# Optimization experiments

Hardware: AMD Instinct MI355X
Metric: run time of the kernel (lower is better)

## Reference

```python
import jax, jax.numpy as jnp
import numpy as np

D_MODEL = 2048
N_HEADS = 32
N_KV = 8
D_HEAD = D_MODEL // N_HEADS  # 64
GROUP = N_HEADS // N_KV      # 4
B, T = 2, 4096
WINDOW = 1024
SINK = 4
ROPE_BASE = 10000.0


def _rope(x, start_pos=0):
    # x: [b, h, t, d]; Llama-style rotate-half RoPE
    t, d = x.shape[2], x.shape[3]
    pos = jnp.arange(start_pos, start_pos + t, dtype=jnp.float32)
    inv_freq = 1.0 / (ROPE_BASE ** (jnp.arange(0, d, 2, dtype=jnp.float32) / d))
    ang = pos[:, None] * inv_freq            # [t, d/2]
    cos, sin = jnp.cos(ang), jnp.sin(ang)
    x1, x2 = jnp.split(x, 2, axis=-1)
    return jnp.concatenate([x1 * cos - x2 * sin, x2 * cos + x1 * sin], axis=-1)


def setup_inputs() -> dict:
    key = jax.random.key(0)
    ks = jax.random.split(key, 5)
    x = jax.random.normal(ks[0], (B, T, D_MODEL), jnp.float32)
    wq = jax.random.normal(ks[1], (D_MODEL, D_MODEL), jnp.float32) * 0.02
    wk = jax.random.normal(ks[2], (N_KV * D_HEAD, D_MODEL), jnp.float32) * 0.02
    wv = jax.random.normal(ks[3], (N_KV * D_HEAD, D_MODEL), jnp.float32) * 0.02
    w_proj = jax.random.normal(ks[4], (D_MODEL, D_MODEL), jnp.float32) * 0.02
    return {"x": x, "wq": wq, "wk": wk, "wv": wv, "w_proj": w_proj}


def reference(x, wq, wk, wv, w_proj):
    b, t, _ = x.shape
    # QKV projections (Linear, no bias): y = x @ W^T, split into heads -> [b,h,t,d]
    q = (x @ wq.T).reshape(b, t, N_HEADS, D_HEAD).transpose(0, 2, 1, 3)
    k = (x @ wk.T).reshape(b, t, N_KV, D_HEAD).transpose(0, 2, 1, 3)
    v = (x @ wv.T).reshape(b, t, N_KV, D_HEAD).transpose(0, 2, 1, 3)
    q = _rope(q, 0)
    k = _rope(k, 0)
    # sliding window + attention sink KV slicing (tokens > window + sink)
    if t > WINDOW + SINK:
        k = jnp.concatenate([k[:, :, :SINK], k[:, :, -WINDOW:]], axis=2)
        v = jnp.concatenate([v[:, :, :SINK], v[:, :, -WINDOW:]], axis=2)
    # repeat_kv: 'b h t d -> b (h group) t d'
    k = jnp.repeat(k, GROUP, axis=1)
    v = jnp.repeat(v, GROUP, axis=1)
    s = k.shape[2]
    scores = jnp.einsum("bhtd,bhsd->bhts", q, k) / np.float32(np.sqrt(D_HEAD))
    # torch SDPA is_causal: top-left aligned tril(L, S)
    causal = jnp.arange(s)[None, :] <= jnp.arange(t)[:, None]  # [t, s]
    scores = jnp.where(causal[None, None], scores, jnp.float32(-1e30))
    probs = jax.nn.softmax(scores, axis=-1)
    ctx = jnp.einsum("bhts,bhsd->bhtd", probs, v)
    ctx = ctx.transpose(0, 2, 1, 3).reshape(b, t, D_MODEL)
    return ctx @ w_proj.T
```

## Files before the change

kernel.cpp:

```cpp
#include <hip/hip_runtime.h>

#define D_MODEL 2048
#define N_HEADS 32
#define N_KV    8
#define D_HEAD  64
#define BATCH   2
#define TLEN    4096
#define WINDOW  1024
#define SINK    4
#define SEQ_S   (WINDOW + SINK)
#define S_PADN  1088
#define MROWS   (BATCH * TLEN)
#define KV_DIM  512
#define KV_STR  1024
#define LOG2E   1.44269504088896340736f
#define PSP     72

typedef __bf16 bf16_t;
typedef __attribute__((ext_vector_type(8))) __bf16 bf16x8;
typedef __attribute__((ext_vector_type(4))) __bf16 bf16x4;
typedef __attribute__((ext_vector_type(4))) float   f32x4;

__device__ __forceinline__ void load_lds16(const void* g, void* l) {
  __builtin_amdgcn_global_load_lds(
      (__attribute__((address_space(1))) void*)g,
      (__attribute__((address_space(3))) void*)l, 16, 0, 0);
}

__global__ __launch_bounds__(256) void cvt_f32_bf16(const float* __restrict__ src,
                                                    bf16_t* __restrict__ dst, int n)
{
  int i = ((int)blockIdx.x * 256 + (int)threadIdx.x) * 4;
  if (i >= n) return;
  const float4 v = *(const float4*)(src + i);
  bf16x4 o;
  o[0] = (bf16_t)v.x; o[1] = (bf16_t)v.y; o[2] = (bf16_t)v.z; o[3] = (bf16_t)v.w;
  *(bf16x4*)(dst + i) = o;
}

template <typename OutT>
__global__ __launch_bounds__(256) void gemm_bt(const bf16_t* __restrict__ A,
                                               const bf16_t* __restrict__ W,
                                               OutT* __restrict__ C,
                                               int M, int N, int K)
{
  __shared__ __align__(16) bf16_t As[128 * 32];
  __shared__ __align__(16) bf16_t Bs[128 * 32];
  const int tid  = threadIdx.x;
  const int lane = tid & 63;
  const int wave = tid >> 6;
  const int quad = lane >> 4;
  const int col  = lane & 15;
  const int wm   = (wave >> 1) * 64;
  const int wn   = (wave & 1) * 64;
  const int bm   = blockIdx.x * 128;
  const int bn   = blockIdx.y * 128;

  const int e0 = tid, e1 = 256 + tid;
  const int r0 = e0 >> 2, c0 = ((e0 & 3) ^ (r0 & 3)) * 8;
  const int r1 = e1 >> 2, c1 = ((e1 & 3) ^ (r1 & 3)) * 8;
  const bf16_t* gA0 = A + (size_t)(bm + r0) * K + c0;
  const bf16_t* gA1 = A + (size_t)(bm + r1) * K + c1;
  const bf16_t* gB0 = W + (size_t)(bn + r0) * K + c0;
  const bf16_t* gB1 = W + (size_t)(bn + r1) * K + c1;
  char* lA0 = (char*)As + wave * 1024;
  char* lA1 = (char*)As + 4096 + wave * 1024;
  char* lB0 = (char*)Bs + wave * 1024;
  char* lB1 = (char*)Bs + 4096 + wave * 1024;

  f32x4 acc[4][4] = {};

  for (int k0 = 0; k0 < K; k0 += 32) {
    __syncthreads();
    load_lds16(gA0 + k0, lA0);
    load_lds16(gA1 + k0, lA1);
    load_lds16(gB0 + k0, lB0);
    load_lds16(gB1 + k0, lB1);
    __syncthreads();
    bf16x8 af[4], bfr[4];
    for (int i = 0; i < 4; ++i) {
      int row = wm + i * 16 + col;
      af[i] = *(const bf16x8*)((const char*)As + row * 64 + ((quad ^ (row & 3)) * 16));
    }
    for (int j = 0; j < 4; ++j) {
      int row = wn + j * 16 + col;
      bfr[j] = *(const bf16x8*)((const char*)Bs + row * 64 + ((quad ^ (row & 3)) * 16));
    }
    for (int i = 0; i < 4; ++i)
      for (int j = 0; j < 4; ++j)
        acc[i][j] = __builtin_amdgcn_mfma_f32_16x16x32_bf16(af[i], bfr[j], acc[i][j], 0, 0, 0);
  }

  for (int i = 0; i < 4; ++i)
    for (int j = 0; j < 4; ++j)
      for (int r = 0; r < 4; ++r) {
        size_t row = (size_t)(bm + wm + i * 16 + quad * 4 + r);
        size_t cc  = (size_t)(bn + wn + j * 16 + col);
        C[row * N + cc] = (OutT)acc[i][j][r];
      }
}

__global__ __launch_bounds__(256) void rope_kernel(bf16_t* __restrict__ q,
                                                   bf16_t* __restrict__ kv)
{
  const size_t QP = (size_t)MROWS * N_HEADS * 32;
  const size_t KP = (size_t)MROWS * N_KV * 32;
  size_t idx = (size_t)blockIdx.x * 256 + threadIdx.x;
  bf16_t* base;
  int i, h, rowlen;
  size_t m;
  if (idx < QP) {
    i = (int)(idx & 31);
    size_t hm = idx >> 5;
    h = (int)(hm & (N_HEADS - 1));
    m = hm >> 5;
    base = q; rowlen = D_MODEL;
  } else {
    idx -= QP;
    if (idx >= KP) return;
    i = (int)(idx & 31);
    size_t hm = idx >> 5;
    h = (int)(hm & (N_KV - 1));
    m = hm >> 3;
    base = kv; rowlen = KV_STR;
  }
  int t = (int)(m & (TLEN - 1));
  float inv = __builtin_exp2f(-(float)i * (13.287712379549449f / 32.0f));
  float ang = (float)t * inv;
  float sn, cs;
  sincosf(ang, &sn, &cs);
  size_t off = m * (size_t)rowlen + (size_t)h * D_HEAD + i;
  float x1 = (float)base[off];
  float x2 = (float)base[off + 32];
  base[off]      = (bf16_t)(x1 * cs - x2 * sn);
  base[off + 32] = (bf16_t)(x2 * cs + x1 * sn);
}

__global__ __launch_bounds__(256) void transpose_v(const bf16_t* __restrict__ KV,
                                                   bf16_t* __restrict__ Vt)
{
  __shared__ __align__(16) bf16_t tile[32][72];
  const int tid = threadIdx.x;
  const int s0  = blockIdx.x * 32;
  const int bk  = blockIdx.y;
  const int b   = bk >> 3, kvh = bk & 7;
  {
    int srow = tid >> 3;
    int dcol = (tid & 7) * 8;
    int sg = s0 + srow;
    int orig = (sg < SINK) ? sg : sg + (TLEN - WINDOW - SINK);
    if (orig > TLEN - 1) orig = TLEN - 1;
    const bf16_t* src = KV + (size_t)(b * TLEN + orig) * KV_STR + KV_DIM + kvh * D_HEAD + dcol;
    *(bf16x8*)&tile[srow][dcol] = *(const bf16x8*)src;
  }
  __syncthreads();
  {
    int d  = tid >> 2;
    int sc = (tid & 3) * 8;
    bf16x8 v;
    for (int j = 0; j < 8; ++j) v[j] = tile[sc + j][d];
    *(bf16x8*)(Vt + (size_t)(bk * 64 + d) * S_PADN + s0 + sc) = v;
  }
}

__global__ __launch_bounds__(256, 3) void attn_kernel(const bf16_t* __restrict__ Q,
                                                      const bf16_t* __restrict__ KV,
                                                      const bf16_t* __restrict__ Vt,
                                                      bf16_t* __restrict__ ctx)
{
  __shared__ __align__(16) bf16_t Ks[2][64 * 64];
  __shared__ __align__(16) bf16_t Vs[2][64 * 64];
  __shared__ __align__(16) bf16_t Ps[4][32 * PSP];
  __shared__ float Lt[4][32];
  const int tid = threadIdx.x, lane = tid & 63, wave = tid >> 6;
  const int quad = lane >> 4, col = lane & 15;
  const int bh = blockIdx.y, b = bh >> 5, h = bh & 31, kvh = h >> 2;
  const int bkv = b * 8 + kvh;
  const int t0b = blockIdx.x * 128;
  const int tw0 = t0b + wave * 32;

  bf16x8 qf[2][2];
  for (int g = 0; g < 2; ++g) {
    const bf16_t* qrow = Q + (size_t)(b * TLEN + tw0 + g * 16 + col) * D_MODEL + h * D_HEAD;
    for (int c = 0; c < 2; ++c) {
      bf16x8 v = *(const bf16x8*)(qrow + c * 32 + quad * 8);
      for (int i = 0; i < 8; ++i) v[i] = (bf16_t)((float)v[i] * (0.125f * LOG2E));
      qf[g][c] = v;
    }
  }

  f32x4 oAcc[2][4] = {};
  float lsum[2] = {0.f, 0.f};

  const int s_end  = (t0b + 128 < SEQ_S) ? t0b + 128 : SEQ_S;
  const int nsteps = (s_end + 63) >> 6;

  auto stage = [&](int st, int buf) {
    const int sb = st * 64;
#pragma unroll
    for (int kk = 0; kk < 2; ++kk) {
      int e = kk * 256 + tid;
      int srow = e >> 3;
      int cb = (e & 7) ^ (srow & 7);
      int sg = sb + srow;
      int orig = (sg < SINK) ? sg : sg + (TLEN - WINDOW - SINK);
      if (orig > TLEN - 1) orig = TLEN - 1;
      const bf16_t* gk = KV + (size_t)(b * TLEN + orig) * KV_STR + kvh * D_HEAD + cb * 8;
      load_lds16(gk, (char*)&Ks[buf][0] + kk * 4096 + wave * 1024);
      const bf16_t* gv = Vt + (size_t)(bkv * 64 + srow) * S_PADN + sb + cb * 8;
      load_lds16(gv, (char*)&Vs[buf][0] + kk * 4096 + wave * 1024);
    }
  };

  stage(0, 0);
  for (int st = 0; st < nsteps; ++st) {
    const int cur = st & 1;
    const int s0 = st * 64;
    const bool dead = (s0 > tw0 + 31);
    const bool full = (s0 + 63 <= tw0) && (s0 + 63 < SEQ_S);
    __syncthreads();

    if (!dead) {
      f32x4 sacc[4][2] = {};
#pragma unroll
      for (int c = 0; c < 2; ++c) {
#pragma unroll
        for (int mt = 0; mt < 4; ++mt) {
          int rr = mt * 16 + col;
          const bf16x8 kf = *(const bf16x8*)((const char*)&Ks[cur][0] + rr * 128 +
                                             ((((c << 2) | quad) ^ (col & 7)) * 16));
          sacc[mt][0] = __builtin_amdgcn_mfma_f32_16x16x32_bf16(kf, qf[0][c], sacc[mt][0], 0, 0, 0);
          sacc[mt][1] = __builtin_amdgcn_mfma_f32_16x16x32_bf16(kf, qf[1][c], sacc[mt][1], 0, 0, 0);
        }
      }
#pragma unroll
      for (int g = 0; g < 2; ++g) {
        const int t = tw0 + g * 16 + col;
#pragma unroll
        for (int mt = 0; mt < 4; ++mt) {
          bf16x4 pk;
          float ls = 0.f;
#pragma unroll
          for (int r = 0; r < 4; ++r) {
            float p = __builtin_exp2f(sacc[mt][g][r]);
            if (!full) {
              int s = s0 + mt * 16 + quad * 4 + r;
              p = (s <= t && s < SEQ_S) ? p : 0.0f;
            }
            ls += p;
            pk[r] = (bf16_t)p;
          }
          lsum[g] += ls;
          *(bf16x4*)(&Ps[wave][(g * 16 + col) * PSP + mt * 16 + quad * 4]) = pk;
        }
      }
    }
    __syncthreads();
    if (st + 1 < nsteps) stage(st + 1, cur ^ 1);

    if (!dead) {
      bf16x8 pf[2][2];
#pragma unroll
      for (int g = 0; g < 2; ++g)
#pragma unroll
        for (int c = 0; c < 2; ++c)
          pf[g][c] = *(const bf16x8*)(&Ps[wave][(g * 16 + col) * PSP + c * 32 + quad * 8]);
#pragma unroll
      for (int c = 0; c < 2; ++c) {
#pragma unroll
        for (int nj = 0; nj < 4; ++nj) {
          int rr = nj * 16 + col;
          const bf16x8 vf = *(const bf16x8*)((const char*)&Vs[cur][0] + rr * 128 +
                                             ((((c << 2) | quad) ^ (col & 7)) * 16));
          oAcc[0][nj] = __builtin_amdgcn_mfma_f32_16x16x32_bf16(pf[0][c], vf, oAcc[0][nj], 0, 0, 0);
          oAcc[1][nj] = __builtin_amdgcn_mfma_f32_16x16x32_bf16(pf[1][c], vf, oAcc[1][nj], 0, 0, 0);
        }
      }
    }
  }

  for (int g = 0; g < 2; ++g) {
    lsum[g] += __shfl_xor(lsum[g], 16, 64);
    lsum[g] += __shfl_xor(lsum[g], 32, 64);
  }
  if (quad == 0) { Lt[wave][col] = lsum[0]; Lt[wave][16 + col] = lsum[1]; }
  __syncthreads();

#pragma unroll
  for (int g = 0; g < 2; ++g) {
    float rli[4];
#pragma unroll
    for (int r = 0; r < 4; ++r)
      rli[r] = __builtin_amdgcn_rcpf(Lt[wave][g * 16 + quad * 4 + r]);
#pragma unroll
    for (int nj = 0; nj < 4; ++nj)
#pragma unroll
      for (int r = 0; r < 4; ++r) {
        size_t row = (size_t)(b * TLEN + tw0 + g * 16 + quad * 4 + r);
        ctx[row * D_MODEL + h * D_HEAD + nj * 16 + col] = (bf16_t)(oAcc[g][nj][r] * rli[r]);
      }
  }
}

extern "C" void kernel_launch(void* const* d_in, const int* in_sizes, int n_in,
                              void* d_out, int out_size, void* d_ws, size_t ws_size,
                              hipStream_t stream)
{
  const float* x  = (const float*)d_in[0];
  const float* wq = (const float*)d_in[1];
  const float* wk = (const float*)d_in[2];
  const float* wv = (const float*)d_in[3];
  const float* wp = (const float*)d_in[4];

  const int NX  = MROWS * D_MODEL;
  const int NWQ = D_MODEL * D_MODEL;
  const int NWK = KV_DIM * D_MODEL;

  bf16_t* xb    = (bf16_t*)d_ws;
  bf16_t* wqb   = xb  + (size_t)NX;
  bf16_t* wkb   = wqb + (size_t)NWQ;
  bf16_t* wvb   = wkb + (size_t)NWK;
  bf16_t* wpb   = wvb + (size_t)NWK;
  bf16_t* q_buf = wpb + (size_t)NWQ;
  bf16_t* kv_buf = q_buf + (size_t)NX;
  bf16_t* vt_buf = kv_buf + (size_t)MROWS * KV_STR;
  bf16_t* c_buf  = xb;
  float*  out    = (float*)d_out;

  cvt_f32_bf16<<<NX  / 1024, 256, 0, stream>>>(x,  xb,  NX);
  cvt_f32_bf16<<<NWQ / 1024, 256, 0, stream>>>(wq, wqb, NWQ);
  cvt_f32_bf16<<<NWK / 1024, 256, 0, stream>>>(wk, wkb, NWK);
  cvt_f32_bf16<<<NWK / 1024, 256, 0, stream>>>(wv, wvb, NWK);
  cvt_f32_bf16<<<NWQ / 1024, 256, 0, stream>>>(wp, wpb, NWQ);

  gemm_bt<bf16_t><<<dim3(MROWS / 128, D_MODEL / 128), 256, 0, stream>>>(xb, wqb, q_buf, MROWS, D_MODEL, D_MODEL);
  gemm_bt<bf16_t><<<dim3(MROWS / 128, KV_STR / 128), 256, 0, stream>>>(xb, wkb, kv_buf, MROWS, KV_STR, D_MODEL);

  {
    size_t total = (size_t)MROWS * N_HEADS * 32 + (size_t)MROWS * N_KV * 32;
    rope_kernel<<<(unsigned)((total + 255) / 256), 256, 0, stream>>>(q_buf, kv_buf);
  }
  transpose_v<<<dim3(S_PADN / 32, BATCH * N_KV), 256, 0, stream>>>(kv_buf, vt_buf);
  attn_kernel<<<dim3(TLEN / 128, BATCH * N_HEADS), 256, 0, stream>>>(q_buf, kv_buf, vt_buf, c_buf);
  gemm_bt<float><<<dim3(MROWS / 128, D_MODEL / 128), 256, 0, stream>>>(c_buf, wpb, out, MROWS, D_MODEL, D_MODEL);
}
```

Measured before the change: 557.7 us.

## Fuse Q RoPE into attention, merge converts, stream V from global

Five fp32-to-bf16 conversion launches are merged into one kernel. Q RoPE moves into the attention kernel's Q-fragment load, so the standalone RoPE pass only touches K. Inside attention, V fragments are read straight from global memory instead of being staged in LDS. The row-sum is computed with an MFMA against a ones vector, which removes the shuffle/LDS reduction and one barrier per step, and occupancy is raised to 4 blocks. The risks are extra sincos work per attention block and uncached global V reads whose latency may not be hidden.

```diff
diff --git a/kernel.cpp b/kernel.cpp
--- a/kernel.cpp
+++ b/kernel.cpp
@@ -27,12 +27,27 @@
       (__attribute__((address_space(3))) void*)l, 16, 0, 0);
 }
 
-__global__ __launch_bounds__(256) void cvt_f32_bf16(const float* __restrict__ src,
-                                                    bf16_t* __restrict__ dst, int n)
-{
-  int i = ((int)blockIdx.x * 256 + (int)threadIdx.x) * 4;
-  if (i >= n) return;
-  const float4 v = *(const float4*)(src + i);
+#define NX  (MROWS * D_MODEL)
+#define NWQ (D_MODEL * D_MODEL)
+#define NWK (KV_DIM * D_MODEL)
+#define NALL (NX + 2 * NWQ + 2 * NWK)
+
+__global__ __launch_bounds__(256) void cvt_all(const float* __restrict__ x,
+                                               const float* __restrict__ wq,
+                                               const float* __restrict__ wk,
+                                               const float* __restrict__ wv,
+                                               const float* __restrict__ wp,
+                                               bf16_t* __restrict__ dst)
+{
+  long i = ((long)blockIdx.x * 256 + threadIdx.x) * 4;
+  const float* src;
+  long off;
+  if (i < NX)                          { src = x;  off = i; }
+  else if (i < NX + NWQ)               { src = wq; off = i - NX; }
+  else if (i < NX + NWQ + NWK)         { src = wk; off = i - NX - NWQ; }
+  else if (i < NX + NWQ + 2L * NWK)    { src = wv; off = i - NX - NWQ - NWK; }
+  else                                 { src = wp; off = i - NX - NWQ - 2L * NWK; }
+  const float4 v = *(const float4*)(src + off);
   bf16x4 o;
   o[0] = (bf16_t)v.x; o[1] = (bf16_t)v.y; o[2] = (bf16_t)v.z; o[3] = (bf16_t)v.w;
   *(bf16x4*)(dst + i) = o;
@@ -100,40 +115,23 @@
       }
 }
 
-__global__ __launch_bounds__(256) void rope_kernel(bf16_t* __restrict__ q,
-                                                   bf16_t* __restrict__ kv)
-{
-  const size_t QP = (size_t)MROWS * N_HEADS * 32;
-  const size_t KP = (size_t)MROWS * N_KV * 32;
+__global__ __launch_bounds__(256) void rope_k(bf16_t* __restrict__ kv)
+{
   size_t idx = (size_t)blockIdx.x * 256 + threadIdx.x;
-  bf16_t* base;
-  int i, h, rowlen;
-  size_t m;
-  if (idx < QP) {
-    i = (int)(idx & 31);
-    size_t hm = idx >> 5;
-    h = (int)(hm & (N_HEADS - 1));
-    m = hm >> 5;
-    base = q; rowlen = D_MODEL;
-  } else {
-    idx -= QP;
-    if (idx >= KP) return;
-    i = (int)(idx & 31);
-    size_t hm = idx >> 5;
-    h = (int)(hm & (N_KV - 1));
-    m = hm >> 3;
-    base = kv; rowlen = KV_STR;
-  }
+  int i = (int)(idx & 31);
+  size_t hm = idx >> 5;
+  int h = (int)(hm & (N_KV - 1));
+  size_t m = hm >> 3;
   int t = (int)(m & (TLEN - 1));
   float inv = __builtin_exp2f(-(float)i * (13.287712379549449f / 32.0f));
   float ang = (float)t * inv;
   float sn, cs;
   sincosf(ang, &sn, &cs);
-  size_t off = m * (size_t)rowlen + (size_t)h * D_HEAD + i;
-  float x1 = (float)base[off];
-  float x2 = (float)base[off + 32];
-  base[off]      = (bf16_t)(x1 * cs - x2 * sn);
-  base[off + 32] = (bf16_t)(x2 * cs + x1 * sn);
+  size_t off = m * (size_t)KV_STR + (size_t)h * D_HEAD + i;
+  float x1 = (float)kv[off];
+  float x2 = (float)kv[off + 32];
+  kv[off]      = (bf16_t)(x1 * cs - x2 * sn);
+  kv[off + 32] = (bf16_t)(x2 * cs + x1 * sn);
 }
 
 __global__ __launch_bounds__(256) void transpose_v(const bf16_t* __restrict__ KV,
@@ -163,15 +161,13 @@
   }
 }
 
-__global__ __launch_bounds__(256, 3) void attn_kernel(const bf16_t* __restrict__ Q,
+__global__ __launch_bounds__(256, 4) void attn_kernel(const bf16_t* __restrict__ Q,
                                                       const bf16_t* __restrict__ KV,
                                                       const bf16_t* __restrict__ Vt,
                                                       bf16_t* __restrict__ ctx)
 {
   __shared__ __align__(16) bf16_t Ks[2][64 * 64];
-  __shared__ __align__(16) bf16_t Vs[2][64 * 64];
   __shared__ __align__(16) bf16_t Ps[4][32 * PSP];
-  __shared__ float Lt[4][32];
   const int tid = threadIdx.x, lane = tid & 63, wave = tid >> 6;
   const int quad = lane >> 4, col = lane & 15;
   const int bh = blockIdx.y, b = bh >> 5, h = bh & 31, kvh = h >> 2;
@@ -180,17 +176,34 @@
   const int tw0 = t0b + wave * 32;
 
   bf16x8 qf[2][2];
-  for (int g = 0; g < 2; ++g) {
-    const bf16_t* qrow = Q + (size_t)(b * TLEN + tw0 + g * 16 + col) * D_MODEL + h * D_HEAD;
-    for (int c = 0; c < 2; ++c) {
-      bf16x8 v = *(const bf16x8*)(qrow + c * 32 + quad * 8);
-      for (int i = 0; i < 8; ++i) v[i] = (bf16_t)((float)v[i] * (0.125f * LOG2E));
-      qf[g][c] = v;
-    }
-  }
+  {
+    float invf[8];
+#pragma unroll
+    for (int jj = 0; jj < 8; ++jj)
+      invf[jj] = __builtin_exp2f(-(float)(quad * 8 + jj) * (13.287712379549449f / 32.0f));
+#pragma unroll
+    for (int g = 0; g < 2; ++g) {
+      const float tpos = (float)(tw0 + g * 16 + col);
+      const bf16_t* qrow = Q + (size_t)(b * TLEN + tw0 + g * 16 + col) * D_MODEL + h * D_HEAD;
+      bf16x8 v0 = *(const bf16x8*)(qrow + quad * 8);
+      bf16x8 v1 = *(const bf16x8*)(qrow + 32 + quad * 8);
+#pragma unroll
+      for (int jj = 0; jj < 8; ++jj) {
+        float sn, cs;
+        sincosf(tpos * invf[jj], &sn, &cs);
+        float x1 = (float)v0[jj], x2 = (float)v1[jj];
+        qf[g][0][jj] = (bf16_t)((x1 * cs - x2 * sn) * (0.125f * LOG2E));
+        qf[g][1][jj] = (bf16_t)((x2 * cs + x1 * sn) * (0.125f * LOG2E));
+      }
+    }
+  }
+
+  bf16x8 ones;
+#pragma unroll
+  for (int j = 0; j < 8; ++j) ones[j] = (bf16_t)1.0f;
 
   f32x4 oAcc[2][4] = {};
-  float lsum[2] = {0.f, 0.f};
+  f32x4 oL[2] = {};
 
   const int s_end  = (t0b + 128 < SEQ_S) ? t0b + 128 : SEQ_S;
   const int nsteps = (s_end + 63) >> 6;
@@ -207,10 +220,10 @@
       if (orig > TLEN - 1) orig = TLEN - 1;
       const bf16_t* gk = KV + (size_t)(b * TLEN + orig) * KV_STR + kvh * D_HEAD + cb * 8;
       load_lds16(gk, (char*)&Ks[buf][0] + kk * 4096 + wave * 1024);
-      const bf16_t* gv = Vt + (size_t)(bkv * 64 + srow) * S_PADN + sb + cb * 8;
-      load_lds16(gv, (char*)&Vs[buf][0] + kk * 4096 + wave * 1024);
     }
   };
+
+  const bf16_t* vbase = Vt + (size_t)(bkv * 64 + col) * S_PADN;
 
   stage(0, 0);
   for (int st = 0; st < nsteps; ++st) {
@@ -219,79 +232,72 @@
     const bool dead = (s0 > tw0 + 31);
     const bool full = (s0 + 63 <= tw0) && (s0 + 63 < SEQ_S);
     __syncthreads();
-
-    if (!dead) {
-      f32x4 sacc[4][2] = {};
+    if (st + 1 < nsteps) stage(st + 1, cur ^ 1);
+
+    if (dead) continue;
+
+    bf16x8 vf0[4];
+#pragma unroll
+    for (int nj = 0; nj < 4; ++nj)
+      vf0[nj] = *(const bf16x8*)(vbase + (size_t)(nj * 16) * S_PADN + s0 + quad * 8);
+
+#pragma unroll
+    for (int mt = 0; mt < 4; ++mt) {
+      const int rr = mt * 16 + col;
+      f32x4 sa0 = {0.f, 0.f, 0.f, 0.f}, sa1 = {0.f, 0.f, 0.f, 0.f};
 #pragma unroll
       for (int c = 0; c < 2; ++c) {
-#pragma unroll
-        for (int mt = 0; mt < 4; ++mt) {
-          int rr = mt * 16 + col;
-          const bf16x8 kf = *(const bf16x8*)((const char*)&Ks[cur][0] + rr * 128 +
-                                             ((((c << 2) | quad) ^ (col & 7)) * 16));
-          sacc[mt][0] = __builtin_amdgcn_mfma_f32_16x16x32_bf16(kf, qf[0][c], sacc[mt][0], 0, 0, 0);
-          sacc[mt][1] = __builtin_amdgcn_mfma_f32_16x16x32_bf16(kf, qf[1][c], sacc[mt][1], 0, 0, 0);
+        const bf16x8 kf = *(const bf16x8*)((const char*)&Ks[cur][0] + rr * 128 +
+                                           ((((c << 2) | quad) ^ (col & 7)) * 16));
+        sa0 = __builtin_amdgcn_mfma_f32_16x16x32_bf16(kf, qf[0][c], sa0, 0, 0, 0);
+        sa1 = __builtin_amdgcn_mfma_f32_16x16x32_bf16(kf, qf[1][c], sa1, 0, 0, 0);
+      }
+#pragma unroll
+      for (int g = 0; g < 2; ++g) {
+        const f32x4 sv = g ? sa1 : sa0;
+        const int t = tw0 + g * 16 + col;
+        bf16x4 pk;
+#pragma unroll
+        for (int r = 0; r < 4; ++r) {
+          float p = __builtin_exp2f(sv[r]);
+          if (!full) {
+            int s = s0 + mt * 16 + quad * 4 + r;
+            p = (s <= t && s < SEQ_S) ? p : 0.0f;
+          }
+          pk[r] = (bf16_t)p;
         }
-      }
-#pragma unroll
-      for (int g = 0; g < 2; ++g) {
-        const int t = tw0 + g * 16 + col;
-#pragma unroll
-        for (int mt = 0; mt < 4; ++mt) {
-          bf16x4 pk;
-          float ls = 0.f;
-#pragma unroll
-          for (int r = 0; r < 4; ++r) {
-            float p = __builtin_exp2f(sacc[mt][g][r]);
-            if (!full) {
-              int s = s0 + mt * 16 + quad * 4 + r;
-              p = (s <= t && s < SEQ_S) ? p : 0.0f;
-            }
-            ls += p;
-            pk[r] = (bf16_t)p;
-          }
-          lsum[g] += ls;
-          *(bf16x4*)(&Ps[wave][(g * 16 + col) * PSP + mt * 16 + quad * 4]) = pk;
-        }
-      }
-    }
-    __syncthreads();
-    if (st + 1 < nsteps) stage(st + 1, cur ^ 1);
-
-    if (!dead) {
-      bf16x8 pf[2][2];
-#pragma unroll
-      for (int g = 0; g < 2; ++g)
-#pragma unroll
-        for (int c = 0; c < 2; ++c)
-          pf[g][c] = *(const bf16x8*)(&Ps[wave][(g * 16 + col) * PSP + c * 32 + quad * 8]);
-#pragma unroll
-      for (int c = 0; c < 2; ++c) {
-#pragma unroll
-        for (int nj = 0; nj < 4; ++nj) {
-          int rr = nj * 16 + col;
-          const bf16x8 vf = *(const bf16x8*)((const char*)&Vs[cur][0] + rr * 128 +
-                                             ((((c << 2) | quad) ^ (col & 7)) * 16));
-          oAcc[0][nj] = __builtin_amdgcn_mfma_f32_16x16x32_bf16(pf[0][c], vf, oAcc[0][nj], 0, 0, 0);
-          oAcc[1][nj] = __builtin_amdgcn_mfma_f32_16x16x32_bf16(pf[1][c], vf, oAcc[1][nj], 0, 0, 0);
-        }
-      }
-    }
-  }
-
-  for (int g = 0; g < 2; ++g) {
-    lsum[g] += __shfl_xor(lsum[g], 16, 64);
-    lsum[g] += __shfl_xor(lsum[g], 32, 64);
-  }
-  if (quad == 0) { Lt[wave][col] = lsum[0]; Lt[wave][16 + col] = lsum[1]; }
-  __syncthreads();
+        *(bf16x4*)(&Ps[wave][(g * 16 + col) * PSP + mt * 16 + quad * 4]) = pk;
+      }
+    }
+
+    bf16x8 vf1[4];
+#pragma unroll
+    for (int nj = 0; nj < 4; ++nj)
+      vf1[nj] = *(const bf16x8*)(vbase + (size_t)(nj * 16) * S_PADN + s0 + 32 + quad * 8);
+
+    __builtin_amdgcn_s_waitcnt(0xC07F);
+
+#pragma unroll
+    for (int c = 0; c < 2; ++c) {
+      bf16x8 pf0 = *(const bf16x8*)(&Ps[wave][(col) * PSP + c * 32 + quad * 8]);
+      bf16x8 pf1 = *(const bf16x8*)(&Ps[wave][(16 + col) * PSP + c * 32 + quad * 8]);
+      oL[0] = __builtin_amdgcn_mfma_f32_16x16x32_bf16(pf0, ones, oL[0], 0, 0, 0);
+      oL[1] = __builtin_amdgcn_mfma_f32_16x16x32_bf16(pf1, ones, oL[1], 0, 0, 0);
+#pragma unroll
+      for (int nj = 0; nj < 4; ++nj) {
+        const bf16x8 vf = c ? vf1[nj] : vf0[nj];
+        oAcc[0][nj] = __builtin_amdgcn_mfma_f32_16x16x32_bf16(pf0, vf, oAcc[0][nj], 0, 0, 0);
+        oAcc[1][nj] = __builtin_amdgcn_mfma_f32_16x16x32_bf16(pf1, vf, oAcc[1][nj], 0, 0, 0);
+      }
+    }
+  }
 
 #pragma unroll
   for (int g = 0; g < 2; ++g) {
     float rli[4];
 #pragma unroll
     for (int r = 0; r < 4; ++r)
-      rli[r] = __builtin_amdgcn_rcpf(Lt[wave][g * 16 + quad * 4 + r]);
+      rli[r] = __builtin_amdgcn_rcpf(oL[g][r]);
 #pragma unroll
     for (int nj = 0; nj < 4; ++nj)
 #pragma unroll
@@ -311,10 +317,6 @@
   const float* wk = (const float*)d_in[2];
   const float* wv = (const float*)d_in[3];
   const float* wp = (const float*)d_in[4];
-
-  const int NX  = MROWS * D_MODEL;
-  const int NWQ = D_MODEL * D_MODEL;
-  const int NWK = KV_DIM * D_MODEL;
 
   bf16_t* xb    = (bf16_t*)d_ws;
   bf16_t* wqb   = xb  + (size_t)NX;
@@ -327,19 +329,12 @@
   bf16_t* c_buf  = xb;
   float*  out    = (float*)d_out;
 
-  cvt_f32_bf16<<<NX  / 1024, 256, 0, stream>>>(x,  xb,  NX);
-  cvt_f32_bf16<<<NWQ / 1024, 256, 0, stream>>>(wq, wqb, NWQ);
-  cvt_f32_bf16<<<NWK / 1024, 256, 0, stream>>>(wk, wkb, NWK);
-  cvt_f32_bf16<<<NWK / 1024, 256, 0, stream>>>(wv, wvb, NWK);
-  cvt_f32_bf16<<<NWQ / 1024, 256, 0, stream>>>(wp, wpb, NWQ);
+  cvt_all<<<NALL / 1024, 256, 0, stream>>>(x, wq, wk, wv, wp, xb);
 
   gemm_bt<bf16_t><<<dim3(MROWS / 128, D_MODEL / 128), 256, 0, stream>>>(xb, wqb, q_buf, MROWS, D_MODEL, D_MODEL);
   gemm_bt<bf16_t><<<dim3(MROWS / 128, KV_STR / 128), 256, 0, stream>>>(xb, wkb, kv_buf, MROWS, KV_STR, D_MODEL);
 
-  {
-    size_t total = (size_t)MROWS * N_HEADS * 32 + (size_t)MROWS * N_KV * 32;
-    rope_kernel<<<(unsigned)((total + 255) / 256), 256, 0, stream>>>(q_buf, kv_buf);
-  }
+  rope_k<<<(MROWS * N_KV * 32) / 256, 256, 0, stream>>>(kv_buf);
   transpose_v<<<dim3(S_PADN / 32, BATCH * N_KV), 256, 0, stream>>>(kv_buf, vt_buf);
   attn_kernel<<<dim3(TLEN / 128, BATCH * N_HEADS), 256, 0, stream>>>(q_buf, kv_buf, vt_buf, c_buf);
   gemm_bt<float><<<dim3(MROWS / 128, D_MODEL / 128), 256, 0, stream>>>(c_buf, wpb, out, MROWS, D_MODEL, D_MODEL);
```

Result: no change. 559.4 us (+0.3%).
